# Kernel optimization log

Hardware: AMD Instinct MI355X
Metric: run time of the kernel (lower is better)

## Reference

```python
import jax, jax.numpy as jnp
import numpy as np

N_PER_G = 6            # EEG channels per graph (complete graph incl. self-loops)
ALPHA = 0.5
BETA1 = float(np.log(1.0 / 1 + 1.0))  # GCN2Conv layer=1, lambda=1
BETA2 = float(np.log(1.0 / 2 + 1.0))  # GCN2Conv layer=2
BN_EPS = 1e-5


def setup_inputs() -> dict:
    key = jax.random.key(0)
    ks = jax.random.split(key, 10)
    G = 400_000
    N = G * N_PER_G          # 2.4M nodes
    E = G * N_PER_G * N_PER_G  # 14.4M edges (complete graph per EEG window)

    x = jax.random.normal(ks[0], (N, 6), dtype=jnp.float32)
    edge_weights = jax.random.uniform(ks[1], (E,), dtype=jnp.float32)

    # Batched complete-graph connectivity (numpy, structured)
    base = (np.arange(G, dtype=np.int64) * N_PER_G)
    ls = np.repeat(np.arange(N_PER_G), N_PER_G)   # local src
    ld = np.tile(np.arange(N_PER_G), N_PER_G)     # local dst
    src = jnp.asarray((base[:, None] + ls[None, :]).reshape(-1).astype(np.int32))
    dst = jnp.asarray((base[:, None] + ld[None, :]).reshape(-1).astype(np.int32))

    s6 = 1.0 / np.sqrt(6.0)
    W1 = jax.random.normal(ks[2], (6, 6), dtype=jnp.float32) * s6
    b1 = jnp.zeros((6,), dtype=jnp.float32)
    W2 = jax.random.normal(ks[3], (6, 6), dtype=jnp.float32) * s6
    b2 = jnp.zeros((6,), dtype=jnp.float32)
    gamma = jnp.ones((6,), dtype=jnp.float32)
    beta_bn = jnp.zeros((6,), dtype=jnp.float32)
    fcW1 = jax.random.normal(ks[4], (6, 10), dtype=jnp.float32) * s6   # xavier-ish
    fcb1 = jnp.zeros((10,), dtype=jnp.float32)
    fcW2 = jax.random.normal(ks[5], (10, 2), dtype=jnp.float32) * (1.0 / np.sqrt(10.0))
    fcb2 = jnp.zeros((2,), dtype=jnp.float32)

    return {"x": x, "edge_weights": edge_weights, "W1": W1, "b1": b1,
            "W2": W2, "b2": b2, "gamma": gamma, "beta_bn": beta_bn,
            "fcW1": fcW1, "fcb1": fcb1, "fcW2": fcW2, "fcb2": fcb2,
            "src": src, "dst": dst, "num_graphs": G}


def _gcn2_conv(feat, feat0, W, b, beta, edge_weights, src, dst, norm, n_nodes):
    # DGL GCN2Conv: sym-norm edge-weighted aggregation, identity mixing, proj mixing
    h = feat * norm                                   # [N,6]
    msg = h[src] * edge_weights[:, None]              # [E,6] gather
    agg = jax.ops.segment_sum(msg, dst, num_segments=n_nodes)  # [N,6] scatter-add
    h = agg * norm
    h = (1.0 - ALPHA) * h + ALPHA * feat0
    return (1.0 - beta) * h + beta * (h @ W) + b


def reference(x, edge_weights, W1, b1, W2, b2, gamma, beta_bn,
              fcW1, fcb1, fcW2, fcb2, src, dst, num_graphs):
    N = x.shape[0]
    # symmetric normalization from in-degrees (clamped to 1)
    deg = jax.ops.segment_sum(jnp.ones_like(edge_weights), dst, num_segments=N)
    norm = jax.lax.rsqrt(jnp.maximum(deg, 1.0))[:, None]  # [N,1]

    h = jax.nn.leaky_relu(_gcn2_conv(x, x, W1, b1, BETA1, edge_weights, src, dst, norm, N))
    h = _gcn2_conv(h, h, W2, b2, BETA2, edge_weights, src, dst, norm, N)

    # BatchNorm1d over nodes (training-mode batch statistics)
    mean = jnp.mean(h, axis=0)
    var = jnp.mean(jnp.square(h - mean), axis=0)
    h = (h - mean) * jax.lax.rsqrt(var + BN_EPS) * gamma + beta_bn
    h = jax.nn.leaky_relu(h)

    # SumPooling per graph (node i belongs to graph i // 6)
    gid = jnp.arange(N, dtype=jnp.int32) // N_PER_G
    pooled = jax.ops.segment_sum(h, gid, num_segments=num_graphs)  # [G,6]

    out = jax.nn.leaky_relu(pooled @ fcW1 + fcb1)  # dropout is identity at inference
    out = out @ fcW2 + fcb2                        # [G,2]
    return out
```

## Files before the change

kernel.cpp:

```cpp
#include <hip/hip_runtime.h>
#include <cstddef>
#include <cstdint>

#define NSLOT 64
#define B1f   0.6931471805599453f
#define B2f   0.4054651081081644f

__device__ __forceinline__ float lrelu(float v) { return v >= 0.0f ? v : 0.01f * v; }

__device__ __forceinline__ unsigned pkbf(float a, float b) {
  unsigned ua = __float_as_uint(a), ub = __float_as_uint(b);
  ua += 0x7FFFu + ((ua >> 16) & 1u);
  ub += 0x7FFFu + ((ub >> 16) & 1u);
  return (ua >> 16) | (ub & 0xFFFF0000u);
}

__device__ __forceinline__ void gl_lds16(const float4* gp, float4* lbase) {
#if __has_builtin(__builtin_amdgcn_global_load_lds)
  __builtin_amdgcn_global_load_lds(
      (const __attribute__((address_space(1))) void*)(const void*)gp,
      (__attribute__((address_space(3))) void*)(void*)lbase, 16, 0, 0);
#else
  ((float4*)lbase)[threadIdx.x & 63] = *gp;
#endif
}

__device__ __forceinline__ void compute_h2_reg(const float xv[36], const float wv[36],
                                               const float* __restrict__ gW1,
                                               const float* __restrict__ gb1,
                                               const float* __restrict__ gW2,
                                               const float* __restrict__ gb2,
                                               float h2[36]) {
  float t[36];
#pragma unroll
  for (int j = 0; j < 6; ++j)
#pragma unroll
    for (int f = 0; f < 6; ++f) {
      float a = 0.f;
#pragma unroll
      for (int i = 0; i < 6; ++i) a = fmaf(wv[i * 6 + j], xv[i * 6 + f], a);
      t[j * 6 + f] = fmaf(a, 1.f / 12.f, 0.5f * xv[j * 6 + f]);
    }
  float h1[36];
#pragma unroll
  for (int j = 0; j < 6; ++j)
#pragma unroll
    for (int f = 0; f < 6; ++f) {
      float a = 0.f;
#pragma unroll
      for (int k = 0; k < 6; ++k) a = fmaf(t[j * 6 + k], gW1[k * 6 + f], a);
      h1[j * 6 + f] = lrelu(fmaf(B1f, a, fmaf(1.f - B1f, t[j * 6 + f], gb1[f])));
    }
#pragma unroll
  for (int j = 0; j < 6; ++j)
#pragma unroll
    for (int f = 0; f < 6; ++f) {
      float a = 0.f;
#pragma unroll
      for (int i = 0; i < 6; ++i) a = fmaf(wv[i * 6 + j], h1[i * 6 + f], a);
      t[j * 6 + f] = fmaf(a, 1.f / 12.f, 0.5f * h1[j * 6 + f]);
    }
#pragma unroll
  for (int j = 0; j < 6; ++j)
#pragma unroll
    for (int f = 0; f < 6; ++f) {
      float a = 0.f;
#pragma unroll
      for (int k = 0; k < 6; ++k) a = fmaf(t[j * 6 + k], gW2[k * 6 + f], a);
      h2[j * 6 + f] = fmaf(B2f, a, fmaf(1.f - B2f, t[j * 6 + f], gb2[f]));
    }
}

__device__ __forceinline__ void bn_coeffs(const float* __restrict__ wsred,
                                          const float* __restrict__ gGamma,
                                          const float* __restrict__ gBeta,
                                          float invN, int lane,
                                          float sc[6], float sh[6]) {
  float st[12];
  const float4* p = reinterpret_cast<const float4*>(wsred) + (size_t)lane * 3;
  float4 a = p[0], b = p[1], c4 = p[2];
  st[0] = a.x;  st[1] = a.y;  st[2]  = a.z;  st[3]  = a.w;
  st[4] = b.x;  st[5] = b.y;  st[6]  = b.z;  st[7]  = b.w;
  st[8] = c4.x; st[9] = c4.y; st[10] = c4.z; st[11] = c4.w;
#pragma unroll
  for (int k = 0; k < 12; ++k)
#pragma unroll
    for (int o = 32; o >= 1; o >>= 1) st[k] += __shfl_xor(st[k], (unsigned)o, 64);
#pragma unroll
  for (int f = 0; f < 6; ++f) {
    float mean = st[f] * invN;
    float var  = st[6 + f] * invN - mean * mean;
    float s    = rsqrtf(var + 1e-5f) * gGamma[f];
    sc[f] = s;
    sh[f] = gBeta[f] - mean * s;
  }
}

__device__ __forceinline__ void pool_fc_out(const float h2[36],
                                            const float sc[6], const float sh[6],
                                            const float* __restrict__ fcW1,
                                            const float* __restrict__ fcb1,
                                            const float* __restrict__ fcW2,
                                            const float* __restrict__ fcb2,
                                            float2* __restrict__ out, int g) {
  float pooled[6] = {0.f, 0.f, 0.f, 0.f, 0.f, 0.f};
#pragma unroll
  for (int j = 0; j < 6; ++j)
#pragma unroll
    for (int f = 0; f < 6; ++f)
      pooled[f] += lrelu(fmaf(h2[j * 6 + f], sc[f], sh[f]));
  float p1[10];
#pragma unroll
  for (int m = 0; m < 10; ++m) {
    float a = fcb1[m];
#pragma unroll
    for (int f = 0; f < 6; ++f) a = fmaf(pooled[f], fcW1[f * 10 + m], a);
    p1[m] = lrelu(a);
  }
  float o0 = fcb2[0], o1 = fcb2[1];
#pragma unroll
  for (int m = 0; m < 10; ++m) {
    o0 = fmaf(p1[m], fcW2[m * 2 + 0], o0);
    o1 = fmaf(p1[m], fcW2[m * 2 + 1], o1);
  }
  out[g] = make_float2(o0, o1);
}

__global__ __launch_bounds__(256, 1) void gcn2_pass1(
    const float* __restrict__ x, const float* __restrict__ ew,
    const float* __restrict__ gW1, const float* __restrict__ gb1,
    const float* __restrict__ gW2, const float* __restrict__ gb2,
    float* __restrict__ wsred, unsigned* __restrict__ h2ws,
    int G, int useWs) {
  __shared__ float4 sbuf[4][2][1152];

  const int tid  = threadIdx.x;
  const int lane = tid & 63;
  const int wid  = tid >> 6;
  const int wgid = blockIdx.x * 4 + wid;
  const int wstr = gridDim.x * 4;
  const int nch  = (G + 63) >> 6;

  const float4* x4 = reinterpret_cast<const float4*>(x);
  const float4* w4 = reinterpret_cast<const float4*>(ew);
  const long fmax4 = (long)G * 9 - 1;

  uint4* wsA = reinterpret_cast<uint4*>(h2ws);
  uint2* wsB = reinterpret_cast<uint2*>(h2ws + (size_t)16 * G);

  float s[6]  = {0.f, 0.f, 0.f, 0.f, 0.f, 0.f};
  float ss[6] = {0.f, 0.f, 0.f, 0.f, 0.f, 0.f};

  int c = wgid;
  if (c < nch) {
    int cur = 0;
#pragma unroll
    for (int k = 0; k < 9; ++k) {
      long fi = (long)c * 576 + k * 64 + lane;
      if (fi > fmax4) fi = fmax4;
      gl_lds16(x4 + fi, &sbuf[wid][0][k * 64]);
    }
#pragma unroll
    for (int k = 0; k < 9; ++k) {
      long fi = (long)c * 576 + k * 64 + lane;
      if (fi > fmax4) fi = fmax4;
      gl_lds16(w4 + fi, &sbuf[wid][0][576 + k * 64]);
    }
    for (;;) {
      const int cn = c + wstr;
      const bool hn = cn < nch;
      if (hn) {
#pragma unroll
        for (int k = 0; k < 9; ++k) {
          long fi = (long)cn * 576 + k * 64 + lane;
          if (fi > fmax4) fi = fmax4;
          gl_lds16(x4 + fi, &sbuf[wid][cur ^ 1][k * 64]);
        }
#pragma unroll
        for (int k = 0; k < 9; ++k) {
          long fi = (long)cn * 576 + k * 64 + lane;
          if (fi > fmax4) fi = fmax4;
          gl_lds16(w4 + fi, &sbuf[wid][cur ^ 1][576 + k * 64]);
        }
      }
      __builtin_amdgcn_sched_barrier(0);
      if (hn) { __asm__ volatile("s_waitcnt vmcnt(18)" ::: "memory"); }
      else    { __asm__ volatile("s_waitcnt vmcnt(0)"  ::: "memory"); }
      __builtin_amdgcn_sched_barrier(0);

      {
        const float4* bx = &sbuf[wid][cur][lane * 9];
        const float4* bw = &sbuf[wid][cur][576 + lane * 9];
        float xv[36], wv[36];
#pragma unroll
        for (int k = 0; k < 9; ++k) {
          float4 v = bx[k];
          xv[4 * k] = v.x; xv[4 * k + 1] = v.y; xv[4 * k + 2] = v.z; xv[4 * k + 3] = v.w;
        }
#pragma unroll
        for (int k = 0; k < 9; ++k) {
          float4 v = bw[k];
          wv[4 * k] = v.x; wv[4 * k + 1] = v.y; wv[4 * k + 2] = v.z; wv[4 * k + 3] = v.w;
        }
#pragma unroll
        for (int q = 0; q < 36; q += 4)
          __asm__ volatile("" : "+v"(xv[q]), "+v"(xv[q + 1]),
                               "+v"(xv[q + 2]), "+v"(xv[q + 3]));
#pragma unroll
        for (int q = 0; q < 36; q += 4)
          __asm__ volatile("" : "+v"(wv[q]), "+v"(wv[q + 1]),
                               "+v"(wv[q + 2]), "+v"(wv[q + 3]));
        __builtin_amdgcn_sched_barrier(0);

        float h2[36];
        compute_h2_reg(xv, wv, gW1, gb1, gW2, gb2, h2);
        const int g = c * 64 + lane;
        if (g < G) {
          if (useWs) {
            unsigned d[18];
#pragma unroll
            for (int k = 0; k < 18; ++k) d[k] = pkbf(h2[2 * k], h2[2 * k + 1]);
            wsA[(size_t)0 * G + g] = make_uint4(d[0],  d[1],  d[2],  d[3]);
            wsA[(size_t)1 * G + g] = make_uint4(d[4],  d[5],  d[6],  d[7]);
            wsA[(size_t)2 * G + g] = make_uint4(d[8],  d[9],  d[10], d[11]);
            wsA[(size_t)3 * G + g] = make_uint4(d[12], d[13], d[14], d[15]);
            wsB[g]                 = make_uint2(d[16], d[17]);
          }
#pragma unroll
          for (int f = 0; f < 6; ++f)
#pragma unroll
            for (int j = 0; j < 6; ++j) {
              float v = h2[j * 6 + f];
              s[f] += v;
              ss[f] = fmaf(v, v, ss[f]);
            }
        }
      }
      if (!hn) break;
      __asm__ volatile("s_waitcnt lgkmcnt(0)" ::: "memory");
      __builtin_amdgcn_sched_barrier(0);
      c = cn;
      cur ^= 1;
    }
  }

#pragma unroll
  for (int f = 0; f < 6; ++f)
#pragma unroll
    for (int o = 32; o >= 1; o >>= 1) {
      s[f]  += __shfl_down(s[f],  (unsigned)o, 64);
      ss[f] += __shfl_down(ss[f], (unsigned)o, 64);
    }
  if (lane == 0) {
    float* p = wsred + (size_t)(wgid & (NSLOT - 1)) * 12;
#pragma unroll
    for (int f = 0; f < 6; ++f) {
      atomicAdd(p + f,     s[f]);
      atomicAdd(p + 6 + f, ss[f]);
    }
  }
}

__global__ __launch_bounds__(256) void gcn2_pass2ws(
    const unsigned* __restrict__ h2ws,
    const float* __restrict__ fcW1, const float* __restrict__ fcb1,
    const float* __restrict__ fcW2, const float* __restrict__ fcb2,
    const float* __restrict__ gGamma, const float* __restrict__ gBeta,
    const float* __restrict__ wsred, float invN,
    float2* __restrict__ out, int G) {
  const int tid  = threadIdx.x;
  const int lane = tid & 63;
  const int g    = blockIdx.x * 256 + tid;

  float sc[6], sh[6];
  bn_coeffs(wsred, gGamma, gBeta, invN, lane, sc, sh);

  if (g >= G) return;

  const uint4* wsA = reinterpret_cast<const uint4*>(h2ws);
  const uint2* wsB = reinterpret_cast<const uint2*>(h2ws + (size_t)16 * G);
  unsigned u[18];
  {
    uint4 a0 = wsA[(size_t)0 * G + g];
    uint4 a1 = wsA[(size_t)1 * G + g];
    uint4 a2 = wsA[(size_t)2 * G + g];
    uint4 a3 = wsA[(size_t)3 * G + g];
    uint2 b0 = wsB[g];
    u[0]=a0.x; u[1]=a0.y; u[2]=a0.z;  u[3]=a0.w;
    u[4]=a1.x; u[5]=a1.y; u[6]=a1.z;  u[7]=a1.w;
    u[8]=a2.x; u[9]=a2.y; u[10]=a2.z; u[11]=a2.w;
    u[12]=a3.x; u[13]=a3.y; u[14]=a3.z; u[15]=a3.w;
    u[16]=b0.x; u[17]=b0.y;
  }
  float h2[36];
#pragma unroll
  for (int d = 0; d < 18; ++d) {
    h2[2 * d]     = __uint_as_float(u[d] << 16);
    h2[2 * d + 1] = __uint_as_float(u[d] & 0xFFFF0000u);
  }
  pool_fc_out(h2, sc, sh, fcW1, fcb1, fcW2, fcb2, out, g);
}

__global__ __launch_bounds__(256) void gcn2_pass2re(
    const float* __restrict__ x, const float* __restrict__ ew,
    const float* __restrict__ gW1, const float* __restrict__ gb1,
    const float* __restrict__ gW2, const float* __restrict__ gb2,
    const float* __restrict__ fcW1, const float* __restrict__ fcb1,
    const float* __restrict__ fcW2, const float* __restrict__ fcb2,
    const float* __restrict__ gGamma, const float* __restrict__ gBeta,
    const float* __restrict__ wsred, float invN,
    float2* __restrict__ out, int G) {
  const int tid  = threadIdx.x;
  const int lane = tid & 63;
  const int g    = blockIdx.x * 256 + tid;

  float sc[6], sh[6];
  bn_coeffs(wsred, gGamma, gBeta, invN, lane, sc, sh);

  if (g >= G) return;

  const float4* px = reinterpret_cast<const float4*>(x)  + (size_t)g * 9;
  const float4* pw = reinterpret_cast<const float4*>(ew) + (size_t)g * 9;
  float xv[36], wv[36];
#pragma unroll
  for (int k = 0; k < 9; ++k) {
    float4 v = px[k];
    xv[4 * k] = v.x; xv[4 * k + 1] = v.y; xv[4 * k + 2] = v.z; xv[4 * k + 3] = v.w;
  }
#pragma unroll
  for (int k = 0; k < 9; ++k) {
    float4 v = pw[k];
    wv[4 * k] = v.x; wv[4 * k + 1] = v.y; wv[4 * k + 2] = v.z; wv[4 * k + 3] = v.w;
  }
  float h2[36];
  compute_h2_reg(xv, wv, gW1, gb1, gW2, gb2, h2);
  pool_fc_out(h2, sc, sh, fcW1, fcb1, fcW2, fcb2, out, g);
}

extern "C" void kernel_launch(void* const* d_in, const int* in_sizes, int n_in,
                              void* d_out, int out_size, void* d_ws, size_t ws_size,
                              hipStream_t stream) {
  const float* x     = (const float*)d_in[0];
  const float* ew    = (const float*)d_in[1];
  const float* W1    = (const float*)d_in[2];
  const float* b1    = (const float*)d_in[3];
  const float* W2    = (const float*)d_in[4];
  const float* b2    = (const float*)d_in[5];
  const float* gamma = (const float*)d_in[6];
  const float* beta  = (const float*)d_in[7];
  const float* fcW1  = (const float*)d_in[8];
  const float* fcb1  = (const float*)d_in[9];
  const float* fcW2  = (const float*)d_in[10];
  const float* fcb2  = (const float*)d_in[11];

  const int G = in_sizes[0] / 36;
  const float invN = 1.0f / (6.0f * (float)G);

  float*    wsred = (float*)d_ws;
  unsigned* h2ws  = (unsigned*)((char*)d_ws + 4096);
  const int useWs = (ws_size >= 4096 + (size_t)G * 72) ? 1 : 0;

  hipMemsetAsync(d_ws, 0, NSLOT * 12 * sizeof(float), stream);

  gcn2_pass1<<<256, 256, 0, stream>>>(x, ew, W1, b1, W2, b2,
                                      wsred, h2ws, G, useWs);
  const int grid2 = (G + 255) / 256;
  if (useWs) {
    gcn2_pass2ws<<<grid2, 256, 0, stream>>>(h2ws, fcW1, fcb1, fcW2, fcb2,
                                            gamma, beta, wsred, invN,
                                            (float2*)d_out, G);
  } else {
    gcn2_pass2re<<<grid2, 256, 0, stream>>>(x, ew, W1, b1, W2, b2,
                                            fcW1, fcb1, fcW2, fcb2,
                                            gamma, beta, wsred, invN,
                                            (float2*)d_out, G);
  }
}
```

Baseline: 52.19 us.

## Prefetch next chunk into registers and single-buffer LDS for two blocks per CU

Replaces the direct global-to-LDS double-buffered loads with register prefetch of the next chunk, which is written into a single LDS buffer after compute. LDS use per block is halved and launch bounds go to 2 blocks per CU, with the grid raised to up to 512 blocks so more waves can hide memory latency. The cost is extra VGPRs for the 18 prefetched float4 values, plus an explicit register-to-LDS copy per iteration. The vmcnt(5) wait counts on the five workspace stores being the only vector-memory ops issued after the prefetch loads, which is fragile. There is also no wait on the LDS writes before the next chunk is read from LDS.

```diff
diff --git a/kernel.cpp b/kernel.cpp
--- a/kernel.cpp
+++ b/kernel.cpp
@@ -13,16 +13,6 @@
   ua += 0x7FFFu + ((ua >> 16) & 1u);
   ub += 0x7FFFu + ((ub >> 16) & 1u);
   return (ua >> 16) | (ub & 0xFFFF0000u);
-}
-
-__device__ __forceinline__ void gl_lds16(const float4* gp, float4* lbase) {
-#if __has_builtin(__builtin_amdgcn_global_load_lds)
-  __builtin_amdgcn_global_load_lds(
-      (const __attribute__((address_space(1))) void*)(const void*)gp,
-      (__attribute__((address_space(3))) void*)(void*)lbase, 16, 0, 0);
-#else
-  ((float4*)lbase)[threadIdx.x & 63] = *gp;
-#endif
 }
 
 __device__ __forceinline__ void compute_h2_reg(const float xv[36], const float wv[36],
@@ -126,13 +116,13 @@
   out[g] = make_float2(o0, o1);
 }
 
-__global__ __launch_bounds__(256, 1) void gcn2_pass1(
+__global__ __launch_bounds__(256, 2) void gcn2_pass1(
     const float* __restrict__ x, const float* __restrict__ ew,
     const float* __restrict__ gW1, const float* __restrict__ gb1,
     const float* __restrict__ gW2, const float* __restrict__ gb2,
     float* __restrict__ wsred, unsigned* __restrict__ h2ws,
     int G, int useWs) {
-  __shared__ float4 sbuf[4][2][1152];
+  __shared__ float4 sbuf[4][1152];
 
   const int tid  = threadIdx.x;
   const int lane = tid & 63;
@@ -151,21 +141,28 @@
   float s[6]  = {0.f, 0.f, 0.f, 0.f, 0.f, 0.f};
   float ss[6] = {0.f, 0.f, 0.f, 0.f, 0.f, 0.f};
 
+  float4 tx[9], tw[9];
+
   int c = wgid;
   if (c < nch) {
-    int cur = 0;
 #pragma unroll
     for (int k = 0; k < 9; ++k) {
       long fi = (long)c * 576 + k * 64 + lane;
       if (fi > fmax4) fi = fmax4;
-      gl_lds16(x4 + fi, &sbuf[wid][0][k * 64]);
+      tx[k] = x4[fi];
     }
 #pragma unroll
     for (int k = 0; k < 9; ++k) {
       long fi = (long)c * 576 + k * 64 + lane;
       if (fi > fmax4) fi = fmax4;
-      gl_lds16(w4 + fi, &sbuf[wid][0][576 + k * 64]);
-    }
+      tw[k] = w4[fi];
+    }
+    __asm__ volatile("s_waitcnt vmcnt(0)" ::: "memory");
+#pragma unroll
+    for (int k = 0; k < 9; ++k) sbuf[wid][k * 64 + lane] = tx[k];
+#pragma unroll
+    for (int k = 0; k < 9; ++k) sbuf[wid][576 + k * 64 + lane] = tw[k];
+
     for (;;) {
       const int cn = c + wstr;
       const bool hn = cn < nch;
@@ -174,23 +171,20 @@
         for (int k = 0; k < 9; ++k) {
           long fi = (long)cn * 576 + k * 64 + lane;
           if (fi > fmax4) fi = fmax4;
-          gl_lds16(x4 + fi, &sbuf[wid][cur ^ 1][k * 64]);
+          tx[k] = x4[fi];
         }
 #pragma unroll
         for (int k = 0; k < 9; ++k) {
           long fi = (long)cn * 576 + k * 64 + lane;
           if (fi > fmax4) fi = fmax4;
-          gl_lds16(w4 + fi, &sbuf[wid][cur ^ 1][576 + k * 64]);
+          tw[k] = w4[fi];
         }
       }
       __builtin_amdgcn_sched_barrier(0);
-      if (hn) { __asm__ volatile("s_waitcnt vmcnt(18)" ::: "memory"); }
-      else    { __asm__ volatile("s_waitcnt vmcnt(0)"  ::: "memory"); }
-      __builtin_amdgcn_sched_barrier(0);
 
       {
-        const float4* bx = &sbuf[wid][cur][lane * 9];
-        const float4* bw = &sbuf[wid][cur][576 + lane * 9];
+        const float4* bx = &sbuf[wid][lane * 9];
+        const float4* bw = &sbuf[wid][576 + lane * 9];
         float xv[36], wv[36];
 #pragma unroll
         for (int k = 0; k < 9; ++k) {
@@ -202,16 +196,6 @@
           float4 v = bw[k];
           wv[4 * k] = v.x; wv[4 * k + 1] = v.y; wv[4 * k + 2] = v.z; wv[4 * k + 3] = v.w;
         }
-#pragma unroll
-        for (int q = 0; q < 36; q += 4)
-          __asm__ volatile("" : "+v"(xv[q]), "+v"(xv[q + 1]),
-                               "+v"(xv[q + 2]), "+v"(xv[q + 3]));
-#pragma unroll
-        for (int q = 0; q < 36; q += 4)
-          __asm__ volatile("" : "+v"(wv[q]), "+v"(wv[q + 1]),
-                               "+v"(wv[q + 2]), "+v"(wv[q + 3]));
-        __builtin_amdgcn_sched_barrier(0);
-
         float h2[36];
         compute_h2_reg(xv, wv, gW1, gb1, gW2, gb2, h2);
         const int g = c * 64 + lane;
@@ -237,10 +221,16 @@
         }
       }
       if (!hn) break;
-      __asm__ volatile("s_waitcnt lgkmcnt(0)" ::: "memory");
+
       __builtin_amdgcn_sched_barrier(0);
+      if (useWs) { __asm__ volatile("s_waitcnt vmcnt(5)" ::: "memory"); }
+      else       { __asm__ volatile("s_waitcnt vmcnt(0)" ::: "memory"); }
+      __builtin_amdgcn_sched_barrier(0);
+#pragma unroll
+      for (int k = 0; k < 9; ++k) sbuf[wid][k * 64 + lane] = tx[k];
+#pragma unroll
+      for (int k = 0; k < 9; ++k) sbuf[wid][576 + k * 64 + lane] = tw[k];
       c = cn;
-      cur ^= 1;
     }
   }
 
@@ -362,8 +352,13 @@
 
   hipMemsetAsync(d_ws, 0, NSLOT * 12 * sizeof(float), stream);
 
-  gcn2_pass1<<<256, 256, 0, stream>>>(x, ew, W1, b1, W2, b2,
-                                      wsred, h2ws, G, useWs);
+  const int nch = (G + 63) / 64;
+  int blocks = (nch + 3) / 4;
+  if (blocks > 512) blocks = 512;
+  if (blocks < 1)   blocks = 1;
+
+  gcn2_pass1<<<blocks, 256, 0, stream>>>(x, ew, W1, b1, W2, b2,
+                                         wsred, h2ws, G, useWs);
   const int grid2 = (G + 255) / 256;
   if (useWs) {
     gcn2_pass2ws<<<grid2, 256, 0, stream>>>(h2ws, fcW1, fcb1, fcW2, fcb2,
```

After: 98.34 us. +88.4%, slower.

## Fuse both passes into one persistent kernel with grid barrier and register-parked h2

Applied to the files above, without the earlier changes.

Replaces the two-kernel flow (pass1 writes bf16 h2 to workspace, pass2 reads it back) with a single persistent kernel of 240 blocks. Each wave keeps its up-to-7 chunks of packed bf16 h2 in registers, publishes BN partial sums, then waits at an atomic grid-wide barrier before applying BN, pooling and the FC layers. This removes the workspace write and re-read plus one kernel launch. In exchange it needs every block co-resident for the spin barrier, and the 126 parked registers per lane add pressure that could cause spills.

```diff
diff --git a/kernel.cpp b/kernel.cpp
--- a/kernel.cpp
+++ b/kernel.cpp
@@ -3,6 +3,9 @@
 #include <cstdint>
 
 #define NSLOT 64
+#define NBLK  240
+#define NWAVE (NBLK * 4)
+#define MAXC  7
 #define B1f   0.6931471805599453f
 #define B2f   0.4054651081081644f
 
@@ -69,6 +72,202 @@
       for (int k = 0; k < 6; ++k) a = fmaf(t[j * 6 + k], gW2[k * 6 + f], a);
       h2[j * 6 + f] = fmaf(B2f, a, fmaf(1.f - B2f, t[j * 6 + f], gb2[f]));
     }
+}
+
+__device__ __forceinline__ void pool_fc_out(const float h2[36],
+                                            const float sc[6], const float sh[6],
+                                            const float* __restrict__ fcW1,
+                                            const float* __restrict__ fcb1,
+                                            const float* __restrict__ fcW2,
+                                            const float* __restrict__ fcb2,
+                                            float2* __restrict__ out, int g) {
+  float pooled[6] = {0.f, 0.f, 0.f, 0.f, 0.f, 0.f};
+#pragma unroll
+  for (int j = 0; j < 6; ++j)
+#pragma unroll
+    for (int f = 0; f < 6; ++f)
+      pooled[f] += lrelu(fmaf(h2[j * 6 + f], sc[f], sh[f]));
+  float p1[10];
+#pragma unroll
+  for (int m = 0; m < 10; ++m) {
+    float a = fcb1[m];
+#pragma unroll
+    for (int f = 0; f < 6; ++f) a = fmaf(pooled[f], fcW1[f * 10 + m], a);
+    p1[m] = lrelu(a);
+  }
+  float o0 = fcb2[0], o1 = fcb2[1];
+#pragma unroll
+  for (int m = 0; m < 10; ++m) {
+    o0 = fmaf(p1[m], fcW2[m * 2 + 0], o0);
+    o1 = fmaf(p1[m], fcW2[m * 2 + 1], o1);
+  }
+  out[g] = make_float2(o0, o1);
+}
+
+__global__ __launch_bounds__(256, 1) void gcn2_fused(
+    const float* __restrict__ x, const float* __restrict__ ew,
+    const float* __restrict__ gW1, const float* __restrict__ gb1,
+    const float* __restrict__ gW2, const float* __restrict__ gb2,
+    const float* __restrict__ fcW1, const float* __restrict__ fcb1,
+    const float* __restrict__ fcW2, const float* __restrict__ fcb2,
+    const float* __restrict__ gGamma, const float* __restrict__ gBeta,
+    float* __restrict__ wsred, int* __restrict__ bar,
+    float2* __restrict__ out, int G, int NB, float invN) {
+  __shared__ float4 sbuf[4][2][1152];
+
+  const int tid  = threadIdx.x;
+  const int lane = tid & 63;
+  const int wid  = tid >> 6;
+  const int wgid = blockIdx.x * 4 + wid;
+  const int nch  = (G + 63) >> 6;
+
+  const float4* x4 = reinterpret_cast<const float4*>(x);
+  const float4* w4 = reinterpret_cast<const float4*>(ew);
+  const long fmax4 = (long)G * 9 - 1;
+
+  float s[6]  = {0.f, 0.f, 0.f, 0.f, 0.f, 0.f};
+  float ss[6] = {0.f, 0.f, 0.f, 0.f, 0.f, 0.f};
+  unsigned park[MAXC][18];
+
+  if (wgid < nch) {
+#pragma unroll
+    for (int k = 0; k < 9; ++k) {
+      long fi = (long)wgid * 576 + k * 64 + lane;
+      if (fi > fmax4) fi = fmax4;
+      gl_lds16(x4 + fi, &sbuf[wid][0][k * 64]);
+    }
+#pragma unroll
+    for (int k = 0; k < 9; ++k) {
+      long fi = (long)wgid * 576 + k * 64 + lane;
+      if (fi > fmax4) fi = fmax4;
+      gl_lds16(w4 + fi, &sbuf[wid][0][576 + k * 64]);
+    }
+  }
+
+  int cur = 0;
+#pragma unroll
+  for (int it = 0; it < MAXC; ++it) {
+    const int c  = wgid + it * NWAVE;
+    const int cn = c + NWAVE;
+    const bool hv = c < nch;
+    const bool hn = cn < nch;
+    if (hn) {
+#pragma unroll
+      for (int k = 0; k < 9; ++k) {
+        long fi = (long)cn * 576 + k * 64 + lane;
+        if (fi > fmax4) fi = fmax4;
+        gl_lds16(x4 + fi, &sbuf[wid][cur ^ 1][k * 64]);
+      }
+#pragma unroll
+      for (int k = 0; k < 9; ++k) {
+        long fi = (long)cn * 576 + k * 64 + lane;
+        if (fi > fmax4) fi = fmax4;
+        gl_lds16(w4 + fi, &sbuf[wid][cur ^ 1][576 + k * 64]);
+      }
+    }
+    __builtin_amdgcn_sched_barrier(0);
+    if (hn) { __asm__ volatile("s_waitcnt vmcnt(18)" ::: "memory"); }
+    else    { __asm__ volatile("s_waitcnt vmcnt(0)"  ::: "memory"); }
+    __builtin_amdgcn_sched_barrier(0);
+
+    if (hv) {
+      const float4* bx = &sbuf[wid][cur][lane * 9];
+      const float4* bw = &sbuf[wid][cur][576 + lane * 9];
+      float xv[36], wv[36];
+#pragma unroll
+      for (int k = 0; k < 9; ++k) {
+        float4 v = bx[k];
+        xv[4 * k] = v.x; xv[4 * k + 1] = v.y; xv[4 * k + 2] = v.z; xv[4 * k + 3] = v.w;
+      }
+#pragma unroll
+      for (int k = 0; k < 9; ++k) {
+        float4 v = bw[k];
+        wv[4 * k] = v.x; wv[4 * k + 1] = v.y; wv[4 * k + 2] = v.z; wv[4 * k + 3] = v.w;
+      }
+      float h2[36];
+      compute_h2_reg(xv, wv, gW1, gb1, gW2, gb2, h2);
+#pragma unroll
+      for (int k = 0; k < 18; ++k) park[it][k] = pkbf(h2[2 * k], h2[2 * k + 1]);
+      const int g = c * 64 + lane;
+      if (g < G) {
+#pragma unroll
+        for (int f = 0; f < 6; ++f)
+#pragma unroll
+          for (int j = 0; j < 6; ++j) {
+            float v = h2[j * 6 + f];
+            s[f] += v;
+            ss[f] = fmaf(v, v, ss[f]);
+          }
+      }
+    } else {
+#pragma unroll
+      for (int k = 0; k < 18; ++k) park[it][k] = 0u;
+    }
+    __asm__ volatile("s_waitcnt lgkmcnt(0)" ::: "memory");
+    __builtin_amdgcn_sched_barrier(0);
+    cur ^= 1;
+  }
+
+#pragma unroll
+  for (int f = 0; f < 6; ++f)
+#pragma unroll
+    for (int o = 32; o >= 1; o >>= 1) {
+      s[f]  += __shfl_down(s[f],  (unsigned)o, 64);
+      ss[f] += __shfl_down(ss[f], (unsigned)o, 64);
+    }
+  if (lane == 0) {
+    float* p = wsred + (size_t)(wgid & (NSLOT - 1)) * 12;
+#pragma unroll
+    for (int f = 0; f < 6; ++f) {
+      atomicAdd(p + f,     s[f]);
+      atomicAdd(p + 6 + f, ss[f]);
+    }
+  }
+  __threadfence();
+  __syncthreads();
+
+  if (tid == 0) {
+    __hip_atomic_fetch_add(bar, 1, __ATOMIC_ACQ_REL, __HIP_MEMORY_SCOPE_AGENT);
+    while (__hip_atomic_load(bar, __ATOMIC_ACQUIRE, __HIP_MEMORY_SCOPE_AGENT) < NB) {
+      __builtin_amdgcn_s_sleep(8);
+    }
+  }
+  __syncthreads();
+
+  float st[12];
+#pragma unroll
+  for (int k = 0; k < 12; ++k)
+    st[k] = __hip_atomic_load(&wsred[lane * 12 + k], __ATOMIC_RELAXED,
+                              __HIP_MEMORY_SCOPE_AGENT);
+#pragma unroll
+  for (int k = 0; k < 12; ++k)
+#pragma unroll
+    for (int o = 32; o >= 1; o >>= 1) st[k] += __shfl_xor(st[k], (unsigned)o, 64);
+  float sc[6], sh[6];
+#pragma unroll
+  for (int f = 0; f < 6; ++f) {
+    float mean = st[f] * invN;
+    float var  = st[6 + f] * invN - mean * mean;
+    float sv   = rsqrtf(var + 1e-5f) * gGamma[f];
+    sc[f] = sv;
+    sh[f] = gBeta[f] - mean * sv;
+  }
+
+#pragma unroll
+  for (int it = 0; it < MAXC; ++it) {
+    const int c = wgid + it * NWAVE;
+    const int g = c * 64 + lane;
+    if (c < nch && g < G) {
+      float h2[36];
+#pragma unroll
+      for (int k = 0; k < 18; ++k) {
+        unsigned u = park[it][k];
+        h2[2 * k]     = __uint_as_float(u << 16);
+        h2[2 * k + 1] = __uint_as_float(u & 0xFFFF0000u);
+      }
+      pool_fc_out(h2, sc, sh, fcW1, fcb1, fcW2, fcb2, out, g);
+    }
+  }
 }
 
 __device__ __forceinline__ void bn_coeffs(const float* __restrict__ wsred,
@@ -96,36 +295,6 @@
   }
 }
 
-__device__ __forceinline__ void pool_fc_out(const float h2[36],
-                                            const float sc[6], const float sh[6],
-                                            const float* __restrict__ fcW1,
-                                            const float* __restrict__ fcb1,
-                                            const float* __restrict__ fcW2,
-                                            const float* __restrict__ fcb2,
-                                            float2* __restrict__ out, int g) {
-  float pooled[6] = {0.f, 0.f, 0.f, 0.f, 0.f, 0.f};
-#pragma unroll
-  for (int j = 0; j < 6; ++j)
-#pragma unroll
-    for (int f = 0; f < 6; ++f)
-      pooled[f] += lrelu(fmaf(h2[j * 6 + f], sc[f], sh[f]));
-  float p1[10];
-#pragma unroll
-  for (int m = 0; m < 10; ++m) {
-    float a = fcb1[m];
-#pragma unroll
-    for (int f = 0; f < 6; ++f) a = fmaf(pooled[f], fcW1[f * 10 + m], a);
-    p1[m] = lrelu(a);
-  }
-  float o0 = fcb2[0], o1 = fcb2[1];
-#pragma unroll
-  for (int m = 0; m < 10; ++m) {
-    o0 = fmaf(p1[m], fcW2[m * 2 + 0], o0);
-    o1 = fmaf(p1[m], fcW2[m * 2 + 1], o1);
-  }
-  out[g] = make_float2(o0, o1);
-}
-
 __global__ __launch_bounds__(256, 1) void gcn2_pass1(
     const float* __restrict__ x, const float* __restrict__ ew,
     const float* __restrict__ gW1, const float* __restrict__ gb1,
@@ -133,24 +302,19 @@
     float* __restrict__ wsred, unsigned* __restrict__ h2ws,
     int G, int useWs) {
   __shared__ float4 sbuf[4][2][1152];
-
   const int tid  = threadIdx.x;
   const int lane = tid & 63;
   const int wid  = tid >> 6;
   const int wgid = blockIdx.x * 4 + wid;
   const int wstr = gridDim.x * 4;
   const int nch  = (G + 63) >> 6;
-
   const float4* x4 = reinterpret_cast<const float4*>(x);
   const float4* w4 = reinterpret_cast<const float4*>(ew);
   const long fmax4 = (long)G * 9 - 1;
-
   uint4* wsA = reinterpret_cast<uint4*>(h2ws);
   uint2* wsB = reinterpret_cast<uint2*>(h2ws + (size_t)16 * G);
-
   float s[6]  = {0.f, 0.f, 0.f, 0.f, 0.f, 0.f};
   float ss[6] = {0.f, 0.f, 0.f, 0.f, 0.f, 0.f};
-
   int c = wgid;
   if (c < nch) {
     int cur = 0;
@@ -187,7 +351,6 @@
       if (hn) { __asm__ volatile("s_waitcnt vmcnt(18)" ::: "memory"); }
       else    { __asm__ volatile("s_waitcnt vmcnt(0)"  ::: "memory"); }
       __builtin_amdgcn_sched_barrier(0);
-
       {
         const float4* bx = &sbuf[wid][cur][lane * 9];
         const float4* bw = &sbuf[wid][cur][576 + lane * 9];
@@ -202,16 +365,6 @@
           float4 v = bw[k];
           wv[4 * k] = v.x; wv[4 * k + 1] = v.y; wv[4 * k + 2] = v.z; wv[4 * k + 3] = v.w;
         }
-#pragma unroll
-        for (int q = 0; q < 36; q += 4)
-          __asm__ volatile("" : "+v"(xv[q]), "+v"(xv[q + 1]),
-                               "+v"(xv[q + 2]), "+v"(xv[q + 3]));
-#pragma unroll
-        for (int q = 0; q < 36; q += 4)
-          __asm__ volatile("" : "+v"(wv[q]), "+v"(wv[q + 1]),
-                               "+v"(wv[q + 2]), "+v"(wv[q + 3]));
-        __builtin_amdgcn_sched_barrier(0);
-
         float h2[36];
         compute_h2_reg(xv, wv, gW1, gb1, gW2, gb2, h2);
         const int g = c * 64 + lane;
@@ -243,7 +396,6 @@
       cur ^= 1;
     }
   }
-
 #pragma unroll
   for (int f = 0; f < 6; ++f)
 #pragma unroll
@@ -271,12 +423,9 @@
   const int tid  = threadIdx.x;
   const int lane = tid & 63;
   const int g    = blockIdx.x * 256 + tid;
-
   float sc[6], sh[6];
   bn_coeffs(wsred, gGamma, gBeta, invN, lane, sc, sh);
-
   if (g >= G) return;
-
   const uint4* wsA = reinterpret_cast<const uint4*>(h2ws);
   const uint2* wsB = reinterpret_cast<const uint2*>(h2ws + (size_t)16 * G);
   unsigned u[18];
@@ -313,12 +462,9 @@
   const int tid  = threadIdx.x;
   const int lane = tid & 63;
   const int g    = blockIdx.x * 256 + tid;
-
   float sc[6], sh[6];
   bn_coeffs(wsred, gGamma, gBeta, invN, lane, sc, sh);
-
   if (g >= G) return;
-
   const float4* px = reinterpret_cast<const float4*>(x)  + (size_t)g * 9;
   const float4* pw = reinterpret_cast<const float4*>(ew) + (size_t)g * 9;
   float xv[36], wv[36];
@@ -353,26 +499,34 @@
   const float* fcW2  = (const float*)d_in[10];
   const float* fcb2  = (const float*)d_in[11];
 
-  const int G = in_sizes[0] / 36;
+  const int G   = in_sizes[0] / 36;
+  const int nch = (G + 63) / 64;
   const float invN = 1.0f / (6.0f * (float)G);
 
-  float*    wsred = (float*)d_ws;
-  unsigned* h2ws  = (unsigned*)((char*)d_ws + 4096);
-  const int useWs = (ws_size >= 4096 + (size_t)G * 72) ? 1 : 0;
-
-  hipMemsetAsync(d_ws, 0, NSLOT * 12 * sizeof(float), stream);
-
-  gcn2_pass1<<<256, 256, 0, stream>>>(x, ew, W1, b1, W2, b2,
-                                      wsred, h2ws, G, useWs);
-  const int grid2 = (G + 255) / 256;
-  if (useWs) {
-    gcn2_pass2ws<<<grid2, 256, 0, stream>>>(h2ws, fcW1, fcb1, fcW2, fcb2,
-                                            gamma, beta, wsred, invN,
-                                            (float2*)d_out, G);
+  float* wsred = (float*)d_ws;
+  int*   bar   = (int*)((char*)d_ws + NSLOT * 12 * 4);
+  hipMemsetAsync(d_ws, 0, NSLOT * 12 * 4 + 64, stream);
+
+  if (nch <= NWAVE * MAXC) {
+    gcn2_fused<<<NBLK, 256, 0, stream>>>(x, ew, W1, b1, W2, b2,
+                                         fcW1, fcb1, fcW2, fcb2,
+                                         gamma, beta, wsred, bar,
+                                         (float2*)d_out, G, NBLK, invN);
   } else {
-    gcn2_pass2re<<<grid2, 256, 0, stream>>>(x, ew, W1, b1, W2, b2,
-                                            fcW1, fcb1, fcW2, fcb2,
-                                            gamma, beta, wsred, invN,
-                                            (float2*)d_out, G);
-  }
-}
+    unsigned* h2ws = (unsigned*)((char*)d_ws + 4096);
+    const int useWs = (ws_size >= 4096 + (size_t)G * 72) ? 1 : 0;
+    gcn2_pass1<<<256, 256, 0, stream>>>(x, ew, W1, b1, W2, b2,
+                                        wsred, h2ws, G, useWs);
+    const int grid2 = (G + 255) / 256;
+    if (useWs) {
+      gcn2_pass2ws<<<grid2, 256, 0, stream>>>(h2ws, fcW1, fcb1, fcW2, fcb2,
+                                              gamma, beta, wsred, invN,
+                                              (float2*)d_out, G);
+    } else {
+      gcn2_pass2re<<<grid2, 256, 0, stream>>>(x, ew, W1, b1, W2, b2,
+                                              fcW1, fcb1, fcW2, fcb2,
+                                              gamma, beta, wsred, invN,
+                                              (float2*)d_out, G);
+    }
+  }
+}
```

Measured after the change: 179.6 us. +244.2%, slower.
